# Kernel optimization log

Hardware: AMD Instinct MI355X
Metric: run time of the kernel (lower is better)

## Reference

```python
import jax, jax.numpy as jnp
import numpy as np


def setup_inputs() -> dict:
    key = jax.random.key(0)
    k1, k2, k3, k4 = jax.random.split(key, 4)
    B, S, D_IN, D_OUT = 4, 2048, 4096, 16384
    inp = jax.random.normal(k1, (B, S, D_IN), dtype=jnp.float32)
    # int8-valued quantized weight stored as int32 (values in [-127, 127])
    quant_w = jax.random.randint(k2, (D_OUT, D_IN), -127, 128, dtype=jnp.int32)
    # per-output-channel scale (weight.abs().max / 127 in the original); keep positive
    scale_w = jax.random.uniform(k3, (D_OUT,), dtype=jnp.float32, minval=0.005, maxval=0.02)
    bias = jax.random.normal(k4, (D_OUT,), dtype=jnp.float32)
    return {"inp": inp, "quant_w": quant_w, "scale_w": scale_w, "bias": bias}


def reference(inp, quant_w, scale_w, bias):
    # extract_weight_to_half (bit_width=8): w_fp = int8_weight * scale[:, None]
    weight = quant_w.astype(scale_w.dtype) * scale_w[:, None]  # [D_OUT, D_IN]
    # W8A16Linear.forward: flatten tokens, mm with weight.T, add bias
    out = jnp.einsum('bsd,od->bso', inp, weight)  # [B, S, D_OUT]
    return out + bias
```

## Files before the change

### kernel.cpp

```cpp
#include <hip/hip_runtime.h>
#include <stdint.h>

typedef __attribute__((ext_vector_type(4))) int iv4;
typedef __attribute__((ext_vector_type(4))) float f32x4;
typedef __attribute__((ext_vector_type(16))) char i8x16;

#define BM 256
#define BN 256
#define BKT 64

__global__ __launch_bounds__(256) void quant_act(const float* __restrict__ in,
                                                 signed char* __restrict__ out,
                                                 float* __restrict__ s_a,
                                                 int K) {
  const int row = blockIdx.x;
  const int t = threadIdx.x;
  const float* a = in + (long)row * K;
  float4 v[4];
#pragma unroll
  for (int i = 0; i < 4; ++i)
    v[i] = reinterpret_cast<const float4*>(a)[t * 4 + i];
  float m = 0.f;
#pragma unroll
  for (int i = 0; i < 4; ++i) {
    m = fmaxf(m, fmaxf(fmaxf(fabsf(v[i].x), fabsf(v[i].y)),
                       fmaxf(fabsf(v[i].z), fabsf(v[i].w))));
  }
#pragma unroll
  for (int off = 32; off; off >>= 1) m = fmaxf(m, __shfl_xor(m, off));
  __shared__ float wmax[4];
  const int lane = t & 63, wvq = t >> 6;
  if (lane == 0) wmax[wvq] = m;
  __syncthreads();
  m = fmaxf(fmaxf(wmax[0], wmax[1]), fmaxf(wmax[2], wmax[3]));
  const float inv = m > 0.f ? 127.f / m : 0.f;
  if (t == 0) s_a[row] = m > 0.f ? m / 127.f : 0.f;
  i8x16 q;
#pragma unroll
  for (int i = 0; i < 4; ++i) {
    q[i * 4 + 0] = (char)(int)rintf(fminf(fmaxf(v[i].x * inv, -127.f), 127.f));
    q[i * 4 + 1] = (char)(int)rintf(fminf(fmaxf(v[i].y * inv, -127.f), 127.f));
    q[i * 4 + 2] = (char)(int)rintf(fminf(fmaxf(v[i].z * inv, -127.f), 127.f));
    q[i * 4 + 3] = (char)(int)rintf(fminf(fmaxf(v[i].w * inv, -127.f), 127.f));
  }
  reinterpret_cast<i8x16*>(out + (long)row * K)[t] = q;
}

__global__ void pack_w(const int* __restrict__ in, signed char* __restrict__ out,
                       long n16) {
  long stride = (long)gridDim.x * blockDim.x;
  for (long i = (long)blockIdx.x * blockDim.x + threadIdx.x; i < n16; i += stride) {
    i8x16 q;
#pragma unroll
    for (int c = 0; c < 4; ++c) {
      int4 w = reinterpret_cast<const int4*>(in)[i * 4 + c];
      q[c * 4 + 0] = (char)w.x;
      q[c * 4 + 1] = (char)w.y;
      q[c * 4 + 2] = (char)w.z;
      q[c * 4 + 3] = (char)w.w;
    }
    reinterpret_cast<i8x16*>(out)[i] = q;
  }
}

#define GLDS16(g, l)                                                          \
  __builtin_amdgcn_global_load_lds(                                           \
      (const __attribute__((address_space(1))) unsigned int*)(g),             \
      (__attribute__((address_space(3))) unsigned int*)(l), 16, 0, 0)

typedef __attribute__((address_space(3))) const signed char lds_c8;

template <int OFF>
__device__ __forceinline__ iv4 ldsb128(lds_c8* p) {
  iv4 r;
  asm volatile("ds_read_b128 %0, %1 offset:%2" : "=v"(r) : "v"(p), "i"(OFF));
  return r;
}

#define BAR __builtin_amdgcn_s_barrier()
#define SCHEDB __builtin_amdgcn_sched_barrier(0)
#define LGKM_0 asm volatile("s_waitcnt lgkmcnt(0)")
#define VMC_4 asm volatile("s_waitcnt vmcnt(4)")

#define MFMA16I(A4, B4, I0)                                                   \
  _Pragma("unroll") for (int i = 0; i < 4; ++i)                               \
    _Pragma("unroll") for (int j = 0; j < 4; ++j)                             \
      acc[(I0) + i][j] = __builtin_amdgcn_mfma_i32_16x16x64_i8(               \
          A4[i], B4[j], acc[(I0) + i][j], 0, 0, 0)

__global__ __launch_bounds__(512, 2) void gemm256_i8(
    const signed char* __restrict__ A,
    const signed char* __restrict__ W,
    const float* __restrict__ s_a,
    const float* __restrict__ scale,
    const float* __restrict__ bias,
    float* __restrict__ C,
    int M, int N, int K) {
  __shared__ __align__(16) signed char As[4][256 * 64];
  __shared__ __align__(16) signed char Bs[4][256 * 64];

  const int tid = threadIdx.x;
  const int lane = tid & 63;
  const int wv = tid >> 6;
  const int wm = wv >> 2;
  const int wn = wv & 3;

  const int nwg = gridDim.x;
  const int bid = blockIdx.x;
  const int wg = ((nwg & 7) == 0) ? ((bid & 7) * (nwg >> 3) + (bid >> 3)) : bid;
  const int mT = M / BM;
  const int bm = wg % mT;
  const int bn = wg / mT;

  const long aRow0 = (long)bm * BM;
  const long wRow0 = (long)bn * BN;

  const int c0 = wv, c1 = 8 + wv;
  const int sr0 = 16 * c0 + (lane >> 2);
  const int sr1 = 16 * c1 + (lane >> 2);
  const int scB = (((lane & 3) ^ ((lane >> 3) & 3))) * 16;
  const signed char* aS0 = A + (aRow0 + sr0) * (long)K + scB;
  const signed char* aS1 = A + (aRow0 + sr1) * (long)K + scB;
  const signed char* wS0 = W + (wRow0 + sr0) * (long)K + scB;
  const signed char* wS1 = W + (wRow0 + sr1) * (long)K + scB;
  const int d0 = c0 * 1024 + lane * 16;
  const int d1 = c1 * 1024 + lane * 16;

  const int sx = (lane >> 4) ^ ((lane >> 1) & 3);
  const int rdA = (wm * 128 + (lane & 15)) * 64 + sx * 16;
  const int rdB = (wn * 64 + (lane & 15)) * 64 + sx * 16;

  iv4 acc[8][4] = {};
  iv4 b[4], a0[4], a1[4];

  const int nk = K / BKT;

  GLDS16(aS0, &As[0][d0]);
  GLDS16(aS1, &As[0][d1]);
  GLDS16(wS0, &Bs[0][d0]);
  GLDS16(wS1, &Bs[0][d1]);
  GLDS16(aS0 + BKT, &As[1][d0]);
  GLDS16(aS1 + BKT, &As[1][d1]);
  GLDS16(wS0 + BKT, &Bs[1][d0]);
  GLDS16(wS1 + BKT, &Bs[1][d1]);

#define TILE_BODY(CUR, STG, KOFF)                                             \
  {                                                                           \
    SCHEDB;                                                                   \
    VMC_4;     \
    BAR;           \
    GLDS16(aS0 + (KOFF), &As[STG][d0]);                                       \
    GLDS16(aS1 + (KOFF), &As[STG][d1]);                                       \
    GLDS16(wS0 + (KOFF), &Bs[STG][d0]);                                       \
    GLDS16(wS1 + (KOFF), &Bs[STG][d1]);                                       \
    SCHEDB;                                                                   \
    {                                                                         \
      lds_c8* pB = (lds_c8*)&Bs[CUR][rdB];                                    \
      lds_c8* pA = (lds_c8*)&As[CUR][rdA];                                    \
      b[0] = ldsb128<0>(pB);    b[1] = ldsb128<1024>(pB);                     \
      b[2] = ldsb128<2048>(pB); b[3] = ldsb128<3072>(pB);                     \
      a0[0] = ldsb128<0>(pA);    a0[1] = ldsb128<1024>(pA);                   \
      a0[2] = ldsb128<2048>(pA); a0[3] = ldsb128<3072>(pA);                   \
      LGKM_0; SCHEDB;                                                         \
      __builtin_amdgcn_s_setprio(1);                                          \
      a1[0] = ldsb128<4096>(pA); a1[1] = ldsb128<5120>(pA);                   \
      a1[2] = ldsb128<6144>(pA); a1[3] = ldsb128<7168>(pA);                   \
      SCHEDB;                                                                 \
      MFMA16I(a0, b, 0);           \
      __builtin_amdgcn_s_setprio(0);                                          \
      SCHEDB; LGKM_0; SCHEDB;                                                 \
      __builtin_amdgcn_s_setprio(1);                                          \
      MFMA16I(a1, b, 4);                                                      \
      __builtin_amdgcn_s_setprio(0);                                          \
    }                                                                         \
    SCHEDB;                                                                   \
  }

  for (int kt = 0; kt < nk; kt += 4) {
    const long ko2 = (long)(kt + 2) * BKT;
    const long ko3 = (long)(kt + 3) * BKT;
    const long ko4 = (kt + 4 < nk) ? (long)(kt + 4) * BKT : 0;
    const long ko5 = (kt + 5 < nk) ? (long)(kt + 5) * BKT : 0;
    TILE_BODY(0, 2, ko2);
    TILE_BODY(1, 3, ko3);
    TILE_BODY(2, 0, ko4);
    TILE_BODY(3, 1, ko5);
  }
#undef TILE_BODY

  const long col0 = wRow0 + wn * 64 + (lane & 15);
  float scl[4], bs[4];
#pragma unroll
  for (int j = 0; j < 4; ++j) {
    scl[j] = scale[col0 + j * 16];
    bs[j] = bias[col0 + j * 16];
  }
  const long row0 = aRow0 + wm * 128 + ((lane >> 4) << 2);
#pragma unroll
  for (int i = 0; i < 8; ++i) {
#pragma unroll
    for (int v = 0; v < 4; ++v) {
      const float rs = s_a[row0 + i * 16 + v];
      float* cp = C + (row0 + i * 16 + v) * (long)N + col0;
#pragma unroll
      for (int j = 0; j < 4; ++j)
        cp[j * 16] = (float)acc[i][j][v] * (rs * scl[j]) + bs[j];
    }
  }
}

__global__ void naive_w8a16(const float* __restrict__ inp,
                            const int* __restrict__ qw,
                            const float* __restrict__ scale,
                            const float* __restrict__ bias,
                            float* __restrict__ out, long M, long N, long K) {
  long idx = (long)blockIdx.x * blockDim.x + threadIdx.x;
  if (idx >= M * N) return;
  long col = idx % N, row = idx / N;
  const float* a = inp + row * K;
  const int* w = qw + col * K;
  float s = 0.f;
  for (long k = 0; k < K; k += 4) {
    float4 av = *reinterpret_cast<const float4*>(&a[k]);
    int4 wv = *reinterpret_cast<const int4*>(&w[k]);
    s += av.x * (float)wv.x + av.y * (float)wv.y + av.z * (float)wv.z +
         av.w * (float)wv.w;
  }
  out[idx] = s * scale[col] + bias[col];
}

extern "C" void kernel_launch(void* const* d_in, const int* in_sizes, int n_in,
                              void* d_out, int out_size, void* d_ws,
                              size_t ws_size, hipStream_t stream) {
  const float* inp = (const float*)d_in[0];
  const int* qw = (const int*)d_in[1];
  const float* scale = (const float*)d_in[2];
  const float* bias = (const float*)d_in[3];
  float* out = (float*)d_out;

  const long N = in_sizes[2];
  const long K = (long)in_sizes[1] / N;
  const long M = (long)in_sizes[0] / K;

  const size_t aB = (size_t)M * K;
  const size_t wB = (size_t)N * K;
  const size_t sB = (size_t)M * 4;
  const long nk = K / BKT;

  if (ws_size >= aB + wB + sB && (M % BM) == 0 && (N % BN) == 0 &&
      K == 4096 && nk >= 8 && (nk % 4) == 0) {
    signed char* Ai8 = (signed char*)d_ws;
    signed char* Wi8 = (signed char*)d_ws + aB;
    float* sA = (float*)((char*)d_ws + aB + wB);
    quant_act<<<(int)M, 256, 0, stream>>>(inp, Ai8, sA, (int)K);
    pack_w<<<2048, 256, 0, stream>>>(qw, Wi8, N * K / 16);
    const int nwg = (int)((M / BM) * (N / BN));
    gemm256_i8<<<nwg, 512, 0, stream>>>(Ai8, Wi8, sA, scale, bias, out,
                                        (int)M, (int)N, (int)K);
  } else {
    long total = M * N;
    naive_w8a16<<<(int)((total + 255) / 256), 256, 0, stream>>>(
        inp, qw, scale, bias, out, M, N, K);
  }
}
```

Before: 778.9 us.

## Double-buffer LDS fragments in registers and interleave MFMA with next-tile reads

Adds two sets of A/B fragment registers so the ds_read_b128 loads for the next K-tile are issued between chunks of MFMAs on the current tile. A prologue now prefetches a third LDS stage and preloads the first fragments. The aim is to hide LDS read latency behind matrix-core work instead of stalling on lgkmcnt before each MFMA block. The cost is 48 extra VGPRs per thread, which under the 512-thread, 2-block launch bound could cause register spills or lower occupancy.

```diff
diff --git a/kernel.cpp b/kernel.cpp
--- a/kernel.cpp
+++ b/kernel.cpp
@@ -2,7 +2,6 @@
 #include <stdint.h>
 
 typedef __attribute__((ext_vector_type(4))) int iv4;
-typedef __attribute__((ext_vector_type(4))) float f32x4;
 typedef __attribute__((ext_vector_type(16))) char i8x16;
 
 #define BM 256
@@ -82,13 +81,13 @@
 #define LGKM_0 asm volatile("s_waitcnt lgkmcnt(0)")
 #define VMC_4 asm volatile("s_waitcnt vmcnt(4)")
 
-#define MFMA16I(A4, B4, I0)                                                   \
+#define MFMA8I(A4, B2, I0, J0)                                                \
   _Pragma("unroll") for (int i = 0; i < 4; ++i)                               \
-    _Pragma("unroll") for (int j = 0; j < 4; ++j)                             \
-      acc[(I0) + i][j] = __builtin_amdgcn_mfma_i32_16x16x64_i8(               \
-          A4[i], B4[j], acc[(I0) + i][j], 0, 0, 0)
-
-__global__ __launch_bounds__(512, 2) void gemm256_i8(
+    _Pragma("unroll") for (int j = 0; j < 2; ++j)                             \
+      acc[(I0) + i][(J0) + j] = __builtin_amdgcn_mfma_i32_16x16x64_i8(        \
+          A4[i], (B2)[j], acc[(I0) + i][(J0) + j], 0, 0, 0)
+
+__global__ __launch_bounds__(512, 2) void gemm256_i8x(
     const signed char* __restrict__ A,
     const signed char* __restrict__ W,
     const float* __restrict__ s_a,
@@ -131,7 +130,8 @@
   const int rdB = (wn * 64 + (lane & 15)) * 64 + sx * 16;
 
   iv4 acc[8][4] = {};
-  iv4 b[4], a0[4], a1[4];
+  iv4 bA[4], a0A[4], a1A[4];
+  iv4 bB[4], a0B[4], a1B[4];
 
   const int nk = K / BKT;
 
@@ -143,48 +143,75 @@
   GLDS16(aS1 + BKT, &As[1][d1]);
   GLDS16(wS0 + BKT, &Bs[1][d0]);
   GLDS16(wS1 + BKT, &Bs[1][d1]);
-
-#define TILE_BODY(CUR, STG, KOFF)                                             \
+  VMC_4;
+  BAR;
+  GLDS16(aS0 + 2 * BKT, &As[2][d0]);
+  GLDS16(aS1 + 2 * BKT, &As[2][d1]);
+  GLDS16(wS0 + 2 * BKT, &Bs[2][d0]);
+  GLDS16(wS1 + 2 * BKT, &Bs[2][d1]);
+  SCHEDB;
+  {
+    lds_c8* pB = (lds_c8*)&Bs[0][rdB];
+    lds_c8* pA = (lds_c8*)&As[0][rdA];
+    bA[0] = ldsb128<0>(pB);    bA[1] = ldsb128<1024>(pB);
+    bA[2] = ldsb128<2048>(pB); bA[3] = ldsb128<3072>(pB);
+    a0A[0] = ldsb128<0>(pA);    a0A[1] = ldsb128<1024>(pA);
+    a0A[2] = ldsb128<2048>(pA); a0A[3] = ldsb128<3072>(pA);
+    a1A[0] = ldsb128<4096>(pA); a1A[1] = ldsb128<5120>(pA);
+    a1A[2] = ldsb128<6144>(pA); a1A[3] = ldsb128<7168>(pA);
+  }
+  LGKM_0; SCHEDB;
+
+#define TILE_BODY(NXTB, STGB, bC, a0C, a1C, bN, a0N, a1N, KOFF)               \
   {                                                                           \
     SCHEDB;                                                                   \
-    VMC_4;     \
-    BAR;           \
-    GLDS16(aS0 + (KOFF), &As[STG][d0]);                                       \
-    GLDS16(aS1 + (KOFF), &As[STG][d1]);                                       \
-    GLDS16(wS0 + (KOFF), &Bs[STG][d0]);                                       \
-    GLDS16(wS1 + (KOFF), &Bs[STG][d1]);                                       \
-    SCHEDB;                                                                   \
+    VMC_4;                 \
+    BAR;              \
+    GLDS16(aS0 + (KOFF), &As[STGB][d0]);                                      \
+    GLDS16(aS1 + (KOFF), &As[STGB][d1]);                                      \
+    GLDS16(wS0 + (KOFF), &Bs[STGB][d0]);                                      \
+    GLDS16(wS1 + (KOFF), &Bs[STGB][d1]);                                      \
+    LGKM_0; SCHEDB;         \
     {                                                                         \
-      lds_c8* pB = (lds_c8*)&Bs[CUR][rdB];                                    \
-      lds_c8* pA = (lds_c8*)&As[CUR][rdA];                                    \
-      b[0] = ldsb128<0>(pB);    b[1] = ldsb128<1024>(pB);                     \
-      b[2] = ldsb128<2048>(pB); b[3] = ldsb128<3072>(pB);                     \
-      a0[0] = ldsb128<0>(pA);    a0[1] = ldsb128<1024>(pA);                   \
-      a0[2] = ldsb128<2048>(pA); a0[3] = ldsb128<3072>(pA);                   \
-      LGKM_0; SCHEDB;                                                         \
-      __builtin_amdgcn_s_setprio(1);                                          \
-      a1[0] = ldsb128<4096>(pA); a1[1] = ldsb128<5120>(pA);                   \
-      a1[2] = ldsb128<6144>(pA); a1[3] = ldsb128<7168>(pA);                   \
-      SCHEDB;                                                                 \
-      MFMA16I(a0, b, 0);           \
-      __builtin_amdgcn_s_setprio(0);                                          \
-      SCHEDB; LGKM_0; SCHEDB;                                                 \
-      __builtin_amdgcn_s_setprio(1);                                          \
-      MFMA16I(a1, b, 4);                                                      \
+      lds_c8* pB = (lds_c8*)&Bs[NXTB][rdB];                                   \
+      lds_c8* pA = (lds_c8*)&As[NXTB][rdA];                                   \
+      __builtin_amdgcn_s_setprio(1);                                          \
+      MFMA8I(a0C, bC + 0, 0, 0);                                              \
+      __builtin_amdgcn_s_setprio(0);                                          \
+      SCHEDB;                                                                 \
+      bN[0] = ldsb128<0>(pB);    bN[1] = ldsb128<1024>(pB);                   \
+      bN[2] = ldsb128<2048>(pB); bN[3] = ldsb128<3072>(pB);                   \
+      SCHEDB;                                                                 \
+      __builtin_amdgcn_s_setprio(1);                                          \
+      MFMA8I(a0C, bC + 2, 0, 2);                                              \
+      __builtin_amdgcn_s_setprio(0);                                          \
+      SCHEDB;                                                                 \
+      a0N[0] = ldsb128<0>(pA);    a0N[1] = ldsb128<1024>(pA);                 \
+      a0N[2] = ldsb128<2048>(pA); a0N[3] = ldsb128<3072>(pA);                 \
+      SCHEDB;                                                                 \
+      __builtin_amdgcn_s_setprio(1);                                          \
+      MFMA8I(a1C, bC + 0, 4, 0);                                              \
+      __builtin_amdgcn_s_setprio(0);                                          \
+      SCHEDB;                                                                 \
+      a1N[0] = ldsb128<4096>(pA); a1N[1] = ldsb128<5120>(pA);                 \
+      a1N[2] = ldsb128<6144>(pA); a1N[3] = ldsb128<7168>(pA);                 \
+      SCHEDB;                                                                 \
+      __builtin_amdgcn_s_setprio(1);                                          \
+      MFMA8I(a1C, bC + 2, 4, 2);                                              \
       __builtin_amdgcn_s_setprio(0);                                          \
     }                                                                         \
     SCHEDB;                                                                   \
   }
 
   for (int kt = 0; kt < nk; kt += 4) {
-    const long ko2 = (long)(kt + 2) * BKT;
     const long ko3 = (long)(kt + 3) * BKT;
     const long ko4 = (kt + 4 < nk) ? (long)(kt + 4) * BKT : 0;
     const long ko5 = (kt + 5 < nk) ? (long)(kt + 5) * BKT : 0;
-    TILE_BODY(0, 2, ko2);
-    TILE_BODY(1, 3, ko3);
-    TILE_BODY(2, 0, ko4);
-    TILE_BODY(3, 1, ko5);
+    const long ko6 = (kt + 6 < nk) ? (long)(kt + 6) * BKT : 0;
+    TILE_BODY(1, 3, bA, a0A, a1A, bB, a0B, a1B, ko3);
+    TILE_BODY(2, 0, bB, a0B, a1B, bA, a0A, a1A, ko4);
+    TILE_BODY(3, 1, bA, a0A, a1A, bB, a0B, a1B, ko5);
+    TILE_BODY(0, 2, bB, a0B, a1B, bA, a0A, a1A, ko6);
   }
 #undef TILE_BODY
 
@@ -255,8 +282,8 @@
     quant_act<<<(int)M, 256, 0, stream>>>(inp, Ai8, sA, (int)K);
     pack_w<<<2048, 256, 0, stream>>>(qw, Wi8, N * K / 16);
     const int nwg = (int)((M / BM) * (N / BN));
-    gemm256_i8<<<nwg, 512, 0, stream>>>(Ai8, Wi8, sA, scale, bias, out,
-                                        (int)M, (int)N, (int)K);
+    gemm256_i8x<<<nwg, 512, 0, stream>>>(Ai8, Wi8, sA, scale, bias, out,
+                                         (int)M, (int)N, (int)K);
   } else {
     long total = M * N;
     naive_w8a16<<<(int)((total + 255) / 256), 256, 0, stream>>>(
```

Measured after the change: 793.2 us. No clear change (+1.8%).

## Restructure int8 GEMM main loop into four-phase pipeline with 128-wide K tiles

Applied to the files above, without the earlier changes.

The int8 GEMM main loop now uses 128-byte K tiles held in a double-buffered LDS layout split into half-tiles. Each K step runs four phases, and each phase interleaves LDS fragment reads and global-to-LDS prefetches with one quarter of the MFMA work, separated by barriers. The aim is to hide LDS and global load latency behind MFMAs and cut the number of barrier-synchronised steps per K. In exchange it adds more barriers per tile and fragile hand-tuned waitcnt and buffer reuse ordering. LDS footprint stays at 128 KB per block.

```diff
diff --git a/kernel.cpp b/kernel.cpp
--- a/kernel.cpp
+++ b/kernel.cpp
@@ -2,12 +2,11 @@
 #include <stdint.h>
 
 typedef __attribute__((ext_vector_type(4))) int iv4;
-typedef __attribute__((ext_vector_type(4))) float f32x4;
 typedef __attribute__((ext_vector_type(16))) char i8x16;
 
 #define BM 256
 #define BN 256
-#define BKT 64
+#define BKB 128
 
 __global__ __launch_bounds__(256) void quant_act(const float* __restrict__ in,
                                                  signed char* __restrict__ out,
@@ -80,15 +79,17 @@
 #define BAR __builtin_amdgcn_s_barrier()
 #define SCHEDB __builtin_amdgcn_sched_barrier(0)
 #define LGKM_0 asm volatile("s_waitcnt lgkmcnt(0)")
+#define LGKM_8 asm volatile("s_waitcnt lgkmcnt(8)")
 #define VMC_4 asm volatile("s_waitcnt vmcnt(4)")
 
-#define MFMA16I(A4, B4, I0)                                                   \
+#define PH_MFMA(AF, BQ, I0, J0)                                               \
   _Pragma("unroll") for (int i = 0; i < 4; ++i)                               \
-    _Pragma("unroll") for (int j = 0; j < 4; ++j)                             \
-      acc[(I0) + i][j] = __builtin_amdgcn_mfma_i32_16x16x64_i8(               \
-          A4[i], B4[j], acc[(I0) + i][j], 0, 0, 0)
-
-__global__ __launch_bounds__(512, 2) void gemm256_i8(
+    _Pragma("unroll") for (int jj = 0; jj < 2; ++jj)                          \
+      _Pragma("unroll") for (int ks = 0; ks < 2; ++ks)                        \
+        acc[(I0) + i][(J0) + jj] = __builtin_amdgcn_mfma_i32_16x16x64_i8(     \
+            AF[i][ks], BQ[jj][ks], acc[(I0) + i][(J0) + jj], 0, 0, 0)
+
+__global__ __launch_bounds__(512, 2) void gemm256_m2(
     const signed char* __restrict__ A,
     const signed char* __restrict__ W,
     const float* __restrict__ s_a,
@@ -96,8 +97,8 @@
     const float* __restrict__ bias,
     float* __restrict__ C,
     int M, int N, int K) {
-  __shared__ __align__(16) signed char As[4][256 * 64];
-  __shared__ __align__(16) signed char Bs[4][256 * 64];
+  __shared__ __align__(16) signed char As[2][2][128 * 128];
+  __shared__ __align__(16) signed char Bs[2][2][128 * 128];
 
   const int tid = threadIdx.x;
   const int lane = tid & 63;
@@ -115,76 +116,97 @@
   const long aRow0 = (long)bm * BM;
   const long wRow0 = (long)bn * BN;
 
-  const int c0 = wv, c1 = 8 + wv;
-  const int sr0 = 16 * c0 + (lane >> 2);
-  const int sr1 = 16 * c1 + (lane >> 2);
-  const int scB = (((lane & 3) ^ ((lane >> 3) & 3))) * 16;
-  const signed char* aS0 = A + (aRow0 + sr0) * (long)K + scB;
-  const signed char* aS1 = A + (aRow0 + sr1) * (long)K + scB;
-  const signed char* wS0 = W + (wRow0 + sr0) * (long)K + scB;
-  const signed char* wS1 = W + (wRow0 + sr1) * (long)K + scB;
-  const int d0 = c0 * 1024 + lane * 16;
-  const int d1 = c1 * 1024 + lane * 16;
-
-  const int sx = (lane >> 4) ^ ((lane >> 1) & 3);
-  const int rdA = (wm * 128 + (lane & 15)) * 64 + sx * 16;
-  const int rdB = (wn * 64 + (lane & 15)) * 64 + sx * 16;
+  const int sRow0 = (0 * 8 + wv) * 8 + (lane >> 3);
+  const int sRow1 = (1 * 8 + wv) * 8 + (lane >> 3);
+  const int srcslot = (lane & 7) ^ (((wv & 1) << 2) | (lane >> 4));
+  const signed char* aS0 = A + (aRow0 + sRow0) * (long)K + srcslot * 16;
+  const signed char* aS1 = A + (aRow0 + sRow1) * (long)K + srcslot * 16;
+  const signed char* wS0 = W + (wRow0 + sRow0) * (long)K + srcslot * 16;
+  const signed char* wS1 = W + (wRow0 + sRow1) * (long)K + srcslot * 16;
+  const long AH = 128 * (long)K;
+  const int d0 = (0 * 8 + wv) * 1024 + lane * 16;
+  const int d1 = (1 * 8 + wv) * 1024 + lane * 16;
+
+  const int rdLane = (lane & 15) * 128 + (((lane >> 4) ^ ((lane >> 1) & 7)) * 16);
+  const int rdB_off = (wn & 1) * 8192;
 
   iv4 acc[8][4] = {};
-  iv4 b[4], a0[4], a1[4];
-
-  const int nk = K / BKT;
-
-  GLDS16(aS0, &As[0][d0]);
-  GLDS16(aS1, &As[0][d1]);
-  GLDS16(wS0, &Bs[0][d0]);
-  GLDS16(wS1, &Bs[0][d1]);
-  GLDS16(aS0 + BKT, &As[1][d0]);
-  GLDS16(aS1 + BKT, &As[1][d1]);
-  GLDS16(wS0 + BKT, &Bs[1][d0]);
-  GLDS16(wS1 + BKT, &Bs[1][d1]);
-
-#define TILE_BODY(CUR, STG, KOFF)                                             \
+  iv4 aF[4][2], bQ0[2][2], bQ1[2][2];
+
+  const int nk = K / BKB;
+
+  GLDS16(aS0, &As[0][0][d0]);           GLDS16(aS1, &As[0][0][d1]);
+  GLDS16(aS0 + AH, &As[0][1][d0]);      GLDS16(aS1 + AH, &As[0][1][d1]);
+  GLDS16(wS0, &Bs[0][0][d0]);           GLDS16(wS1, &Bs[0][0][d1]);
+  GLDS16(wS0 + AH, &Bs[0][1][d0]);      GLDS16(wS1 + AH, &Bs[0][1][d1]);
+  GLDS16(wS0 + AH + BKB, &Bs[1][1][d0]); GLDS16(wS1 + AH + BKB, &Bs[1][1][d1]);
+  GLDS16(aS0 + BKB, &As[1][0][d0]);     GLDS16(aS1 + BKB, &As[1][0][d1]);
+  VMC_4;
+  BAR;
+
+#define TILE_BODY(CUR, NXT, KO1, KO2)                                         \
   {                                                                           \
-    SCHEDB;                                                                   \
-    VMC_4;     \
-    BAR;           \
-    GLDS16(aS0 + (KOFF), &As[STG][d0]);                                       \
-    GLDS16(aS1 + (KOFF), &As[STG][d1]);                                       \
-    GLDS16(wS0 + (KOFF), &Bs[STG][d0]);                                       \
-    GLDS16(wS1 + (KOFF), &Bs[STG][d1]);                                       \
-    SCHEDB;                                                                   \
-    {                                                                         \
-      lds_c8* pB = (lds_c8*)&Bs[CUR][rdB];                                    \
-      lds_c8* pA = (lds_c8*)&As[CUR][rdA];                                    \
-      b[0] = ldsb128<0>(pB);    b[1] = ldsb128<1024>(pB);                     \
-      b[2] = ldsb128<2048>(pB); b[3] = ldsb128<3072>(pB);                     \
-      a0[0] = ldsb128<0>(pA);    a0[1] = ldsb128<1024>(pA);                   \
-      a0[2] = ldsb128<2048>(pA); a0[3] = ldsb128<3072>(pA);                   \
-      LGKM_0; SCHEDB;                                                         \
-      __builtin_amdgcn_s_setprio(1);                                          \
-      a1[0] = ldsb128<4096>(pA); a1[1] = ldsb128<5120>(pA);                   \
-      a1[2] = ldsb128<6144>(pA); a1[3] = ldsb128<7168>(pA);                   \
-      SCHEDB;                                                                 \
-      MFMA16I(a0, b, 0);           \
-      __builtin_amdgcn_s_setprio(0);                                          \
-      SCHEDB; LGKM_0; SCHEDB;                                                 \
-      __builtin_amdgcn_s_setprio(1);                                          \
-      MFMA16I(a1, b, 4);                                                      \
-      __builtin_amdgcn_s_setprio(0);                                          \
-    }                                                                         \
-    SCHEDB;                                                                   \
-  }
-
-  for (int kt = 0; kt < nk; kt += 4) {
-    const long ko2 = (long)(kt + 2) * BKT;
-    const long ko3 = (long)(kt + 3) * BKT;
-    const long ko4 = (kt + 4 < nk) ? (long)(kt + 4) * BKT : 0;
-    const long ko5 = (kt + 5 < nk) ? (long)(kt + 5) * BKT : 0;
-    TILE_BODY(0, 2, ko2);
-    TILE_BODY(1, 3, ko3);
-    TILE_BODY(2, 0, ko4);
-    TILE_BODY(3, 1, ko5);
+    lds_c8* pAk0 = (lds_c8*)&As[CUR][wm][rdLane];                             \
+    lds_c8* pAk1 = (lds_c8*)&As[CUR][wm][rdLane ^ 64];                        \
+    lds_c8* pBk0 = (lds_c8*)&Bs[CUR][wn >> 1][rdB_off + rdLane];              \
+    lds_c8* pBk1 = (lds_c8*)&Bs[CUR][wn >> 1][rdB_off + (rdLane ^ 64)];       \
+                                    \
+    bQ0[0][0] = ldsb128<0>(pBk0);    bQ0[0][1] = ldsb128<0>(pBk1);            \
+    bQ0[1][0] = ldsb128<2048>(pBk0); bQ0[1][1] = ldsb128<2048>(pBk1);         \
+    aF[0][0] = ldsb128<0>(pAk0);     aF[0][1] = ldsb128<0>(pAk1);             \
+    aF[1][0] = ldsb128<2048>(pAk0);  aF[1][1] = ldsb128<2048>(pAk1);          \
+    aF[2][0] = ldsb128<4096>(pAk0);  aF[2][1] = ldsb128<4096>(pAk1);          \
+    aF[3][0] = ldsb128<6144>(pAk0);  aF[3][1] = ldsb128<6144>(pAk1);          \
+    GLDS16(aS0 + AH + (KO1), &As[NXT][1][d0]);                                \
+    GLDS16(aS1 + AH + (KO1), &As[NXT][1][d1]);                                \
+    LGKM_8; SCHEDB;                                                           \
+    BAR;                                                                      \
+    LGKM_0; SCHEDB;                                                           \
+    __builtin_amdgcn_s_setprio(1);                                            \
+    PH_MFMA(aF, bQ0, 0, 0);                                                   \
+    __builtin_amdgcn_s_setprio(0);                                            \
+    SCHEDB; BAR;                                                              \
+                                     \
+    bQ1[0][0] = ldsb128<4096>(pBk0); bQ1[0][1] = ldsb128<4096>(pBk1);         \
+    bQ1[1][0] = ldsb128<6144>(pBk0); bQ1[1][1] = ldsb128<6144>(pBk1);         \
+    GLDS16(wS0 + (KO1), &Bs[NXT][0][d0]);                                     \
+    GLDS16(wS1 + (KO1), &Bs[NXT][0][d1]);                                     \
+    BAR;                                                                      \
+    LGKM_0; SCHEDB;                                                           \
+    __builtin_amdgcn_s_setprio(1);                                            \
+    PH_MFMA(aF, bQ1, 0, 2);                                                   \
+    __builtin_amdgcn_s_setprio(0);                                            \
+    SCHEDB; BAR;                                                              \
+                                     \
+    aF[0][0] = ldsb128<8192>(pAk0);  aF[0][1] = ldsb128<8192>(pAk1);          \
+    aF[1][0] = ldsb128<10240>(pAk0); aF[1][1] = ldsb128<10240>(pAk1);         \
+    aF[2][0] = ldsb128<12288>(pAk0); aF[2][1] = ldsb128<12288>(pAk1);         \
+    aF[3][0] = ldsb128<14336>(pAk0); aF[3][1] = ldsb128<14336>(pAk1);         \
+    GLDS16(wS0 + AH + (KO2), &Bs[CUR][1][d0]);                                \
+    GLDS16(wS1 + AH + (KO2), &Bs[CUR][1][d1]);                                \
+    BAR;                                                                      \
+    LGKM_0; SCHEDB;                                                           \
+    __builtin_amdgcn_s_setprio(1);                                            \
+    PH_MFMA(aF, bQ1, 4, 2);                                                   \
+    __builtin_amdgcn_s_setprio(0);                                            \
+    SCHEDB; BAR;                                                              \
+      \
+    GLDS16(aS0 + (KO2), &As[CUR][0][d0]);                                     \
+    GLDS16(aS1 + (KO2), &As[CUR][0][d1]);                                     \
+    __builtin_amdgcn_s_setprio(1);                                            \
+    PH_MFMA(aF, bQ0, 4, 0);                                                   \
+    __builtin_amdgcn_s_setprio(0);                                            \
+    VMC_4; SCHEDB;                                                            \
+    BAR;                                                                      \
+  }
+
+  for (int kt = 0; kt < nk; kt += 2) {
+    const long ka1 = (long)(kt + 1) * BKB;
+    const long ka2 = (kt + 2 < nk) ? (long)(kt + 2) * BKB : 0;
+    const long kb1 = ka2;
+    const long kb2 = (kt + 3 < nk) ? (long)(kt + 3) * BKB : 0;
+    TILE_BODY(0, 1, ka1, ka2);
+    TILE_BODY(1, 0, kb1, kb2);
   }
 #undef TILE_BODY
 
@@ -245,17 +267,17 @@
   const size_t aB = (size_t)M * K;
   const size_t wB = (size_t)N * K;
   const size_t sB = (size_t)M * 4;
-  const long nk = K / BKT;
+  const long nk = K / BKB;
 
   if (ws_size >= aB + wB + sB && (M % BM) == 0 && (N % BN) == 0 &&
-      K == 4096 && nk >= 8 && (nk % 4) == 0) {
+      K == 4096 && nk >= 4 && (nk % 2) == 0) {
     signed char* Ai8 = (signed char*)d_ws;
     signed char* Wi8 = (signed char*)d_ws + aB;
     float* sA = (float*)((char*)d_ws + aB + wB);
     quant_act<<<(int)M, 256, 0, stream>>>(inp, Ai8, sA, (int)K);
     pack_w<<<2048, 256, 0, stream>>>(qw, Wi8, N * K / 16);
     const int nwg = (int)((M / BM) * (N / BN));
-    gemm256_i8<<<nwg, 512, 0, stream>>>(Ai8, Wi8, sA, scale, bias, out,
+    gemm256_m2<<<nwg, 512, 0, stream>>>(Ai8, Wi8, sA, scale, bias, out,
                                         (int)M, (int)N, (int)K);
   } else {
     long total = M * N;
```

After: 694.0 us. -10.9%, faster.
